# Performance work log

Measured on AMD Instinct MI355X. Metric: run time of the kernel, lower is better.

Reference implementation:

```python
import jax, jax.numpy as jnp
import numpy as np

B, N, R = 16, 128, 16256
OBJ_D, REL_D, EFF_D = 64, 32, 100
REL_HID, OBJ_HID = 150, 100


def setup_inputs() -> dict:
    key = jax.random.key(0)
    ks = jax.random.split(key, 20)
    inp = {
        "objects": jax.random.normal(ks[0], (B, N, OBJ_D), jnp.float32),
        "sender_relations": jax.random.uniform(ks[1], (B, N, R), jnp.float32),
        "receiver_relations": jax.random.uniform(ks[2], (B, N, R), jnp.float32),
        "relation_info": jax.random.normal(ks[3], (B, R, REL_D), jnp.float32),
    }
    rel_in = 2 * OBJ_D + REL_D  # 160
    def lin(k, fin, fout):
        s = 1.0 / np.sqrt(fin)
        kw, kb = jax.random.split(k)
        w = jax.random.uniform(kw, (fin, fout), jnp.float32, -s, s)
        b = jax.random.uniform(kb, (fout,), jnp.float32, -s, s)
        return w, b
    inp["rw1"], inp["rb1"] = lin(ks[4], rel_in, REL_HID)
    inp["rw2"], inp["rb2"] = lin(ks[5], REL_HID, REL_HID)
    inp["rw3"], inp["rb3"] = lin(ks[6], REL_HID, REL_HID)
    inp["rw4"], inp["rb4"] = lin(ks[7], REL_HID, EFF_D)
    inp["ow1"], inp["ob1"] = lin(ks[8], OBJ_D + EFF_D, OBJ_HID)
    inp["ow2"], inp["ob2"] = lin(ks[9], OBJ_HID, 1)
    return inp


def reference(objects, sender_relations, receiver_relations, relation_info,
              rw1, rb1, rw2, rb2, rw3, rb3, rw4, rb4, ow1, ob1, ow2, ob2):
    # gather: [B,R,N] @ [B,N,D] -> [B,R,D]
    senders = jnp.einsum("bnr,bnd->brd", sender_relations, objects)
    receivers = jnp.einsum("bnr,bnd->brd", receiver_relations, objects)
    x = jnp.concatenate([senders, receivers, relation_info], axis=2)  # [B,R,160]
    h = jax.nn.relu(x @ rw1 + rb1)
    h = jax.nn.relu(h @ rw2 + rb2)
    h = jax.nn.relu(h @ rw3 + rb3)
    effects = jax.nn.relu(h @ rw4 + rb4)  # [B,R,EFF_D]
    # scatter: [B,N,R] @ [B,R,E] -> [B,N,E]
    effect_receivers = jnp.einsum("bnr,bre->bne", receiver_relations, effects)
    y = jnp.concatenate([objects, effect_receivers], axis=2)  # [B,N,OBJ_D+EFF_D]
    y = y.reshape(-1, y.shape[-1])  # [B*N, 164]
    predicted = jax.nn.relu(y @ ow1 + ob1) @ ow2 + ob2  # [B*N, 1]
    return jax.nn.sigmoid(predicted)
```

## Files before the change

### kernel.cpp

```cpp
#include <hip/hip_runtime.h>
#include <math.h>

#define B_    16
#define N_    128
#define R_    16256
#define OBJD  64
#define RELD  32
#define EFFD  100
#define HID   150
#define MT    64
#define NTILE (R_ / MT)

typedef __bf16 bf16x8 __attribute__((ext_vector_type(8)));
typedef float  f32x4  __attribute__((ext_vector_type(4)));
typedef unsigned int  uint4v __attribute__((ext_vector_type(4)));
typedef unsigned short u16;
typedef unsigned long long u64;

#define MFMA(a,b,c) (c) = __builtin_amdgcn_mfma_f32_16x16x32_bf16((a), (b), (c), 0, 0, 0)

#define EF_FLOATS (B_*N_*EFFD)
#define A1_ELEMS  (B_*160*288)
#define W2_ELEMS  (160*160)
#define W4_ELEMS  (128*160)
#define U_A1H 0
#define U_A1L (U_A1H + A1_ELEMS)
#define U_W2H (U_A1L + A1_ELEMS)
#define U_W2L (U_W2H + W2_ELEMS)
#define U_W3H (U_W2L + W2_ELEMS)
#define U_W3L (U_W3H + W2_ELEMS)
#define U_W4H (U_W3L + W2_ELEMS)
#define U_W4L (U_W4H + W4_ELEMS)

__device__ __forceinline__ u16 bfh(float x){
    unsigned u = __float_as_uint(x);
    return (u16)((u + 0x7FFFu + ((u >> 16) & 1u)) >> 16);
}
__device__ __forceinline__ float bff(u16 h){ return __uint_as_float(((unsigned)h) << 16); }
__device__ __forceinline__ void split2(float x, u16 &h, u16 &l){
    h = bfh(x);
    l = bfh(x - bff(h));
}
__device__ __forceinline__ u64 pack4(const u16 h[4]){
    return (u64)((unsigned)h[0] | ((unsigned)h[1] << 16))
         | ((u64)((unsigned)h[2] | ((unsigned)h[3] << 16)) << 32);
}

__global__ __launch_bounds__(128) void k0a(const float* __restrict__ obj,
                                           const float* __restrict__ rw1,
                                           u16* __restrict__ A1H, u16* __restrict__ A1L){
    const int j = blockIdx.x;
    const int b = blockIdx.y;
    const int n = threadIdx.x;
    float s = 0.f, rc = 0.f;
    if (j < HID){
        const float* o = obj + ((size_t)b*N_ + n)*OBJD;
#pragma unroll
        for (int d = 0; d < OBJD; ++d){
            const float ov = o[d];
            s  += ov * rw1[d*HID + j];
            rc += ov * rw1[(OBJD + d)*HID + j];
        }
    }
    const size_t base = ((size_t)b*160 + j)*288;
    const int pos = (n & ~31) + (((((n >> 3) & 3) ^ (j & 3))) << 3) + (n & 7);
    u16 h, l;
    split2(s, h, l);  A1H[base + pos] = h;        A1L[base + pos] = l;
    split2(rc, h, l); A1H[base + 128 + pos] = h;  A1L[base + 128 + pos] = l;
    if (n < RELD){
        const float v = (j < HID) ? rw1[(2*OBJD + n)*HID + j] : 0.f;
        const int p2 = 256 + ((((n >> 3) & 3) ^ (j & 3)) << 3) + (n & 7);
        split2(v, h, l); A1H[base + p2] = h; A1L[base + p2] = l;
    }
}

__global__ __launch_bounds__(160) void k0b(const float* __restrict__ rw2,
                                           const float* __restrict__ rw3,
                                           const float* __restrict__ rw4,
                                           u16* W2H, u16* W2L, u16* W3H, u16* W3L,
                                           u16* W4H, u16* W4L){
    const int out = blockIdx.x;
    const int m   = blockIdx.y;
    const int k   = threadIdx.x;
    const int pos = (k & ~31) + ((((k >> 3) & 3) ^ (out & 3)) << 3) + (k & 7);
    u16 h, l;
    if (m == 2){
        if (out >= 128) return;
        const float v = (out < EFFD && k < HID) ? rw4[k*EFFD + out] : 0.f;
        split2(v, h, l);
        W4H[out*160 + pos] = h; W4L[out*160 + pos] = l;
    } else {
        const float* W = (m == 0) ? rw2 : rw3;
        u16* DH = (m == 0) ? W2H : W3H;
        u16* DL = (m == 0) ? W2L : W3L;
        const float v = (out < HID && k < HID) ? W[k*HID + out] : 0.f;
        split2(v, h, l);
        DH[out*160 + pos] = h; DL[out*160 + pos] = l;
    }
}

#define ACT_H 0
#define ACT_L 20480
#define WA_H  40960
#define WA_L  51200
#define BS_H  61440
#define BS_L  65536
#define RRE_H 0
#define RRE_L 20480
#define EFF_H 40960
#define EFF_L 61440
#define SMEM_BYTES 81920

__global__ __launch_bounds__(256, 2) void k1(
    const float* __restrict__ SR, const float* __restrict__ RR, const float* __restrict__ REL,
    const float* __restrict__ rb1, const float* __restrict__ rb2,
    const float* __restrict__ rb3, const float* __restrict__ rb4,
    const u16* __restrict__ UA, float* __restrict__ EF){

    __shared__ __align__(16) unsigned char smem[SMEM_BYTES];

    const int t    = threadIdx.x;
    const int wid  = t >> 6;
    const int lane = t & 63;
    const int lr   = lane & 15;
    const int lg   = lane >> 4;
    const int wr   = wid >> 1;
    const int wc   = wid & 1;
    const int b    = blockIdx.y;
    const int r0   = blockIdx.x * MT;

    const u16* A1Hb = UA + U_A1H + (size_t)b*160*288;
    const u16* A1Lb = UA + U_A1L + (size_t)b*160*288;

    u64 wh[5], wl[5];
    float bsv[8];

    auto wload = [&](const u16* GH, const u16* GL, int KW, int pieces, int c){
#pragma unroll
        for (int q = 0; q < 5; ++q){
            const int p = t + 256*q;
            if (p < pieces){
                const size_t off = (size_t)(p >> 3)*KW + c*32 + (p & 7)*4;
                wh[q] = *(const u64*)(GH + off);
                wl[q] = *(const u64*)(GL + off);
            }
        }
    };
    auto wwrite = [&](int pieces){
#pragma unroll
        for (int q = 0; q < 5; ++q){
            const int p = t + 256*q;
            if (p < pieces){
                *(u64*)(smem + WA_H + p*8) = wh[q];
                *(u64*)(smem + WA_L + p*8) = wl[q];
            }
        }
    };
    auto bs_load_srr = [&](int c){
        const float* SRC = (c < 4) ? SR : RR;
        const float* base = SRC + ((size_t)b*N_ + (c & 3)*32 + wid*8)*R_ + r0 + lane;
#pragma unroll
        for (int q = 0; q < 8; ++q) bsv[q] = base[(size_t)q * R_];
    };
    auto bs_load_rel = [&](){
        const int rel = t >> 2, gq = t & 3;
        const float* src = REL + ((size_t)b*R_ + r0 + rel)*RELD + gq*8;
#pragma unroll
        for (int q = 0; q < 8; ++q) bsv[q] = src[q];
    };
    auto bs_pack_write = [&](int rel, int gr){
        unsigned ph[4], pl[4];
#pragma unroll
        for (int i = 0; i < 4; ++i){
            u16 h0, l0, h1, l1;
            split2(bsv[2*i],   h0, l0);
            split2(bsv[2*i+1], h1, l1);
            ph[i] = (unsigned)h0 | ((unsigned)h1 << 16);
            pl[i] = (unsigned)l0 | ((unsigned)l1 << 16);
        }
        const int off = (rel*4 + (gr ^ (rel & 3))) * 16;
        uint4v H; H[0]=ph[0]; H[1]=ph[1]; H[2]=ph[2]; H[3]=ph[3];
        uint4v L; L[0]=pl[0]; L[1]=pl[1]; L[2]=pl[2]; L[3]=pl[3];
        *(uint4v*)(smem + BS_H + off) = H;
        *(uint4v*)(smem + BS_L + off) = L;
    };
    auto RD = [&](int off) -> bf16x8 {
        return __builtin_bit_cast(bf16x8, *(const uint4v*)(smem + off));
    };

    f32x4 acc[5][2];

    auto epi_act = [&](){
#pragma unroll
        for (int mb = 0; mb < 5; ++mb){
            const int out0 = wr*80 + mb*16 + lg*4;
            const int g = out0 >> 3;
#pragma unroll
            for (int nb = 0; nb < 2; ++nb){
                const int rel = wc*32 + nb*16 + lr;
                const int g2 = (g & ~3) | ((g & 3) ^ (rel & 3));
                u16 h[4], l[4];
#pragma unroll
                for (int r = 0; r < 4; ++r){
                    const float v = fmaxf(acc[mb][nb][r], 0.f);
                    split2(v, h[r], l[r]);
                }
                const int ob = (rel*20 + g2)*16 + (out0 & 7)*2;
                *(u64*)(smem + ACT_H + ob) = pack4(h);
                *(u64*)(smem + ACT_L + ob) = pack4(l);
            }
        }
    };

    {
#pragma unroll
        for (int mb = 0; mb < 5; ++mb){
            const int o0 = wr*80 + mb*16 + lg*4;
            f32x4 bv;
#pragma unroll
            for (int r = 0; r < 4; ++r) bv[r] = (o0 + r < HID) ? rb1[o0 + r] : 0.f;
            acc[mb][0] = bv; acc[mb][1] = bv;
        }
        wload(A1Hb, A1Lb, 288, 1280, 0);
        bs_load_srr(0);
        wwrite(1280);
        bs_pack_write(lane, wid);
        __syncthreads();
        for (int c = 0; c < 9; ++c){
            if (c < 8){
                wload(A1Hb, A1Lb, 288, 1280, c + 1);
                if (c + 1 < 8) bs_load_srr(c + 1); else bs_load_rel();
            }
            bf16x8 ah[5], al[5], bh[2], bl[2];
#pragma unroll
            for (int mb = 0; mb < 5; ++mb){
                const int row = wr*80 + mb*16 + lr;
                const int off = (row*4 + (lg ^ (row & 3))) * 16;
                ah[mb] = RD(WA_H + off); al[mb] = RD(WA_L + off);
            }
#pragma unroll
            for (int nb = 0; nb < 2; ++nb){
                const int rel = wc*32 + nb*16 + lr;
                const int off = (rel*4 + (lg ^ (rel & 3))) * 16;
                bh[nb] = RD(BS_H + off); bl[nb] = RD(BS_L + off);
            }
            __syncthreads();
#pragma unroll
            for (int mb = 0; mb < 5; ++mb)
#pragma unroll
            for (int nb = 0; nb < 2; ++nb){
                MFMA(ah[mb], bh[nb], acc[mb][nb]);
                MFMA(ah[mb], bl[nb], acc[mb][nb]);
                MFMA(al[mb], bh[nb], acc[mb][nb]);
            }
            if (c < 8){
                wwrite(1280);
                if (c + 1 < 8) bs_pack_write(lane, wid); else bs_pack_write(t >> 2, t & 3);
            }
            __syncthreads();
        }
        epi_act();
        __syncthreads();
    }

    {
        const u16* WHs[2] = { UA + U_W2H, UA + U_W3H };
        const u16* WLs[2] = { UA + U_W2L, UA + U_W3L };
        const float* RBs[2] = { rb2, rb3 };
        for (int L = 0; L < 2; ++L){
#pragma unroll
            for (int mb = 0; mb < 5; ++mb){
                const int o0 = wr*80 + mb*16 + lg*4;
                f32x4 bv;
#pragma unroll
                for (int r = 0; r < 4; ++r) bv[r] = (o0 + r < HID) ? RBs[L][o0 + r] : 0.f;
                acc[mb][0] = bv; acc[mb][1] = bv;
            }
            wload(WHs[L], WLs[L], 160, 1280, 0);
            wwrite(1280);
            __syncthreads();
            for (int c = 0; c < 5; ++c){
                if (c < 4) wload(WHs[L], WLs[L], 160, 1280, c + 1);
                bf16x8 ah[5], al[5], bh[2], bl[2];
#pragma unroll
                for (int mb = 0; mb < 5; ++mb){
                    const int row = wr*80 + mb*16 + lr;
                    const int off = (row*4 + (lg ^ (row & 3))) * 16;
                    ah[mb] = RD(WA_H + off); al[mb] = RD(WA_L + off);
                }
#pragma unroll
                for (int nb = 0; nb < 2; ++nb){
                    const int rel = wc*32 + nb*16 + lr;
                    const int off = (rel*20 + c*4 + (lg ^ (rel & 3))) * 16;
                    bh[nb] = RD(ACT_H + off); bl[nb] = RD(ACT_L + off);
                }
                __syncthreads();
#pragma unroll
                for (int mb = 0; mb < 5; ++mb)
#pragma unroll
                for (int nb = 0; nb < 2; ++nb){
                    MFMA(ah[mb], bh[nb], acc[mb][nb]);
                    MFMA(ah[mb], bl[nb], acc[mb][nb]);
                    MFMA(al[mb], bh[nb], acc[mb][nb]);
                }
                if (c < 4) wwrite(1280);
                __syncthreads();
            }
            epi_act();
            __syncthreads();
        }
    }

    {
        f32x4 a4[2][4];
#pragma unroll
        for (int eb = 0; eb < 4; ++eb){
            const int e = wc*64 + eb*16 + lr;
            const float bvv = (e < EFFD) ? rb4[e] : 0.f;
            f32x4 v; v[0]=bvv; v[1]=bvv; v[2]=bvv; v[3]=bvv;
            a4[0][eb] = v; a4[1][eb] = v;
        }
        float vrr[32];
        {
            const int n = t >> 1, half = t & 1;
            const float* src = RR + ((size_t)b*N_ + n)*R_ + r0 + half*32;
#pragma unroll
            for (int q = 0; q < 8; ++q){
                const float4 f = *(const float4*)(src + q*4);
                vrr[q*4+0] = f.x; vrr[q*4+1] = f.y; vrr[q*4+2] = f.z; vrr[q*4+3] = f.w;
            }
        }
        const u16* W4Hp = UA + U_W4H;
        const u16* W4Lp = UA + U_W4L;
        wload(W4Hp, W4Lp, 160, 1024, 0);
        wwrite(1024);
        __syncthreads();
        for (int c = 0; c < 5; ++c){
            if (c < 4) wload(W4Hp, W4Lp, 160, 1024, c + 1);
            bf16x8 ah[2], al[2], bh[4], bl[4];
#pragma unroll
            for (int rb = 0; rb < 2; ++rb){
                const int row = wr*32 + rb*16 + lr;
                const int off = (row*20 + c*4 + (lg ^ (row & 3))) * 16;
                ah[rb] = RD(ACT_H + off); al[rb] = RD(ACT_L + off);
            }
#pragma unroll
            for (int eb = 0; eb < 4; ++eb){
                const int row = wc*64 + eb*16 + lr;
                const int off = (row*4 + (lg ^ (row & 3))) * 16;
                bh[eb] = RD(WA_H + off); bl[eb] = RD(WA_L + off);
            }
            __syncthreads();
#pragma unroll
            for (int rb = 0; rb < 2; ++rb)
#pragma unroll
            for (int eb = 0; eb < 4; ++eb){
                MFMA(ah[rb], bh[eb], a4[rb][eb]);
                MFMA(ah[rb], bl[eb], a4[rb][eb]);
                MFMA(al[rb], bh[eb], a4[rb][eb]);
            }
            if (c < 4) wwrite(1024);
            __syncthreads();
        }
#pragma unroll
        for (int rb = 0; rb < 2; ++rb){
            const int rel0 = wr*32 + rb*16 + lg*4;
            const int g = rel0 >> 3;
#pragma unroll
            for (int eb = 0; eb < 4; ++eb){
                const int e = wc*64 + eb*16 + lr;
                const int g2 = (g & ~3) | ((g & 3) ^ (e & 3));
                u16 h[4], l[4];
#pragma unroll
                for (int r = 0; r < 4; ++r){
                    const float v = fmaxf(a4[rb][eb][r], 0.f);
                    split2(v, h[r], l[r]);
                }
                const int ob = (e*10 + g2)*16 + (rel0 & 7)*2;
                *(u64*)(smem + EFF_H + ob) = pack4(h);
                *(u64*)(smem + EFF_L + ob) = pack4(l);
            }
        }
        {
            const int n = t >> 1, half = t & 1;
#pragma unroll
            for (int gq = 0; gq < 4; ++gq){
                unsigned ph[4], pl[4];
#pragma unroll
                for (int i = 0; i < 4; ++i){
                    u16 h0, l0, h1, l1;
                    split2(vrr[gq*8 + 2*i],     h0, l0);
                    split2(vrr[gq*8 + 2*i + 1], h1, l1);
                    ph[i] = (unsigned)h0 | ((unsigned)h1 << 16);
                    pl[i] = (unsigned)l0 | ((unsigned)l1 << 16);
                }
                const int off = (n*10 + half*4 + (gq ^ (n & 3))) * 16;
                uint4v H; H[0]=ph[0]; H[1]=ph[1]; H[2]=ph[2]; H[3]=ph[3];
                uint4v L; L[0]=pl[0]; L[1]=pl[1]; L[2]=pl[2]; L[3]=pl[3];
                *(uint4v*)(smem + RRE_H + off) = H;
                *(uint4v*)(smem + RRE_L + off) = L;
            }
        }
        __syncthreads();
    }

    {
        f32x4 ae[4][4];
#pragma unroll
        for (int nb = 0; nb < 4; ++nb)
#pragma unroll
        for (int eb = 0; eb < 4; ++eb){
            ae[nb][eb][0]=0.f; ae[nb][eb][1]=0.f; ae[nb][eb][2]=0.f; ae[nb][eb][3]=0.f;
        }
#pragma unroll
        for (int ks = 0; ks < 2; ++ks){
            bf16x8 rh[4], rl[4], eh[4], el[4];
#pragma unroll
            for (int nb = 0; nb < 4; ++nb){
                const int row = wr*64 + nb*16 + lr;
                const int off = (row*10 + ks*4 + (lg ^ (row & 3))) * 16;
                rh[nb] = RD(RRE_H + off); rl[nb] = RD(RRE_L + off);
            }
#pragma unroll
            for (int eb = 0; eb < 4; ++eb){
                const int row = wc*64 + eb*16 + lr;
                const int off = (row*10 + ks*4 + (lg ^ (row & 3))) * 16;
                eh[eb] = RD(EFF_H + off); el[eb] = RD(EFF_L + off);
            }
#pragma unroll
            for (int nb = 0; nb < 4; ++nb)
#pragma unroll
            for (int eb = 0; eb < 4; ++eb){
                MFMA(rh[nb], eh[eb], ae[nb][eb]);
                MFMA(rh[nb], el[eb], ae[nb][eb]);
                MFMA(rl[nb], eh[eb], ae[nb][eb]);
            }
        }
        float* EFb = EF + (size_t)b*N_*EFFD;
#pragma unroll
        for (int eb = 0; eb < 4; ++eb){
            const int e = wc*64 + eb*16 + lr;
            if (e < EFFD){
#pragma unroll
                for (int nb = 0; nb < 4; ++nb){
                    const int n0 = wr*64 + nb*16 + lg*4;
#pragma unroll
                    for (int r = 0; r < 4; ++r)
                        atomicAdd(&EFb[(size_t)(n0 + r)*EFFD + e], ae[nb][eb][r]);
                }
            }
        }
    }
}

__global__ __launch_bounds__(128) void k3_out(
    const float* __restrict__ EF, const float* __restrict__ obj,
    const float* __restrict__ ow1, const float* __restrict__ ob1,
    const float* __restrict__ ow2, const float* __restrict__ ob2,
    float* __restrict__ out) {
    __shared__ float y[OBJD + EFFD];
    __shared__ float red[128];
    const int bn = blockIdx.x;
    const int t  = threadIdx.x;
    if (t < OBJD) y[t] = obj[(size_t)bn * OBJD + t];
    if (t < EFFD) y[OBJD + t] = EF[(size_t)bn * EFFD + t];
    __syncthreads();
    float prod = 0.f;
    if (t < 100) {
        float h = ob1[t];
#pragma unroll
        for (int k = 0; k < OBJD + EFFD; ++k) h += y[k] * ow1[k * 100 + t];
        prod = fmaxf(h, 0.f) * ow2[t];
    }
    red[t] = prod;
    __syncthreads();
#pragma unroll
    for (int s = 64; s > 0; s >>= 1) {
        if (t < s) red[t] += red[t + s];
        __syncthreads();
    }
    if (t == 0) {
        const float x = red[0] + ob2[0];
        float sig;
        if (x >= 0.f) sig = 1.f / (1.f + expf(-x));
        else { const float e = expf(x); sig = e / (1.f + e); }
        out[bn] = sig;
    }
}

extern "C" void kernel_launch(void* const* d_in, const int* in_sizes, int n_in,
                              void* d_out, int out_size, void* d_ws, size_t ws_size,
                              hipStream_t stream) {
    const float* obj = (const float*)d_in[0];
    const float* SR  = (const float*)d_in[1];
    const float* RR  = (const float*)d_in[2];
    const float* REL = (const float*)d_in[3];
    const float* rw1 = (const float*)d_in[4];
    const float* rb1 = (const float*)d_in[5];
    const float* rw2 = (const float*)d_in[6];
    const float* rb2 = (const float*)d_in[7];
    const float* rw3 = (const float*)d_in[8];
    const float* rb3 = (const float*)d_in[9];
    const float* rw4 = (const float*)d_in[10];
    const float* rb4 = (const float*)d_in[11];
    const float* ow1 = (const float*)d_in[12];
    const float* ob1 = (const float*)d_in[13];
    const float* ow2 = (const float*)d_in[14];
    const float* ob2 = (const float*)d_in[15];
    float* out = (float*)d_out;
    float* ws  = (float*)d_ws;

    float* EF = ws;
    u16*   UA = (u16*)(ws + EF_FLOATS);

    hipMemsetAsync(EF, 0, (size_t)EF_FLOATS * sizeof(float), stream);

    k0a<<<dim3(160, B_), dim3(128), 0, stream>>>(obj, rw1, UA + U_A1H, UA + U_A1L);
    k0b<<<dim3(160, 3), dim3(160), 0, stream>>>(rw2, rw3, rw4,
                                                UA + U_W2H, UA + U_W2L,
                                                UA + U_W3H, UA + U_W3L,
                                                UA + U_W4H, UA + U_W4L);
    k1<<<dim3(NTILE, B_), dim3(256), 0, stream>>>(SR, RR, REL, rb1, rb2, rb3, rb4,
                                                  (const u16*)UA, EF);
    k3_out<<<dim3(B_ * N_), dim3(128), 0, stream>>>(EF, obj, ow1, ob1, ow2, ob2, out);
}
```

Baseline: 800.9 us.

## Double-buffer weight and operand LDS tiles and retune XOR swizzle patterns

Weight and relation-operand staging buffers in shared memory become two ping-pong buffers per GEMM stage, so the barrier between reading fragments and writing the next chunk is dropped, leaving one sync per k-step. The swizzle functions also change from XOR with row&3 to XOR with (row>>1)&3 or (row>>2)&3, which is meant to cut LDS bank conflicts for the row strides used. The risk is more LDS layout pressure within the existing 80 KB footprint, plus the correctness of reusing the ACT/EFF regions once the extra barriers are gone.

```diff
diff --git a/kernel.cpp b/kernel.cpp
--- a/kernel.cpp
+++ b/kernel.cpp
@@ -18,6 +18,9 @@
 typedef unsigned long long u64;
 
 #define MFMA(a,b,c) (c) = __builtin_amdgcn_mfma_f32_16x16x32_bf16((a), (b), (c), 0, 0, 0)
+
+#define SWZA(r,g) ((g) ^ (((r) >> 1) & 3))
+#define SWZE(r,g) ((g) ^ (((r) >> 2) & 3))
 
 #define EF_FLOATS (B_*N_*EFFD)
 #define A1_ELEMS  (B_*160*288)
@@ -63,13 +66,13 @@
         }
     }
     const size_t base = ((size_t)b*160 + j)*288;
-    const int pos = (n & ~31) + (((((n >> 3) & 3) ^ (j & 3))) << 3) + (n & 7);
+    const int pos = (n & ~31) + (SWZA(j, (n >> 3) & 3) << 3) + (n & 7);
     u16 h, l;
     split2(s, h, l);  A1H[base + pos] = h;        A1L[base + pos] = l;
     split2(rc, h, l); A1H[base + 128 + pos] = h;  A1L[base + 128 + pos] = l;
     if (n < RELD){
         const float v = (j < HID) ? rw1[(2*OBJD + n)*HID + j] : 0.f;
-        const int p2 = 256 + ((((n >> 3) & 3) ^ (j & 3)) << 3) + (n & 7);
+        const int p2 = 256 + (SWZA(j, (n >> 3) & 3) << 3) + (n & 7);
         split2(v, h, l); A1H[base + p2] = h; A1L[base + p2] = l;
     }
 }
@@ -82,7 +85,7 @@
     const int out = blockIdx.x;
     const int m   = blockIdx.y;
     const int k   = threadIdx.x;
-    const int pos = (k & ~31) + ((((k >> 3) & 3) ^ (out & 3)) << 3) + (k & 7);
+    const int pos = (k & ~31) + (SWZA(out, (k >> 3) & 3) << 3) + (k & 7);
     u16 h, l;
     if (m == 2){
         if (out >= 128) return;
@@ -99,12 +102,12 @@
     }
 }
 
+#define G1WB(i) ((i) * 20480)
+#define G1BS(i) (61440 + (i) * 8192)
 #define ACT_H 0
 #define ACT_L 20480
-#define WA_H  40960
-#define WA_L  51200
-#define BS_H  61440
-#define BS_L  65536
+#define G2WB(i) (40960 + (i) * 20480)
+#define G4WB(i) (40960 + (i) * 16384)
 #define RRE_H 0
 #define RRE_L 20480
 #define EFF_H 40960
@@ -146,13 +149,14 @@
             }
         }
     };
-    auto wwrite = [&](int pieces){
+    auto wwrite = [&](int base, int pieces){
+        const int loff = pieces * 8;
 #pragma unroll
         for (int q = 0; q < 5; ++q){
             const int p = t + 256*q;
             if (p < pieces){
-                *(u64*)(smem + WA_H + p*8) = wh[q];
-                *(u64*)(smem + WA_L + p*8) = wl[q];
+                *(u64*)(smem + base + p*8)        = wh[q];
+                *(u64*)(smem + base + loff + p*8) = wl[q];
             }
         }
     };
@@ -168,7 +172,7 @@
 #pragma unroll
         for (int q = 0; q < 8; ++q) bsv[q] = src[q];
     };
-    auto bs_pack_write = [&](int rel, int gr){
+    auto bs_pack_write = [&](int base, int rel, int gr){
         unsigned ph[4], pl[4];
 #pragma unroll
         for (int i = 0; i < 4; ++i){
@@ -178,11 +182,11 @@
             ph[i] = (unsigned)h0 | ((unsigned)h1 << 16);
             pl[i] = (unsigned)l0 | ((unsigned)l1 << 16);
         }
-        const int off = (rel*4 + (gr ^ (rel & 3))) * 16;
+        const int off = (rel*4 + SWZA(rel, gr)) * 16;
         uint4v H; H[0]=ph[0]; H[1]=ph[1]; H[2]=ph[2]; H[3]=ph[3];
         uint4v L; L[0]=pl[0]; L[1]=pl[1]; L[2]=pl[2]; L[3]=pl[3];
-        *(uint4v*)(smem + BS_H + off) = H;
-        *(uint4v*)(smem + BS_L + off) = L;
+        *(uint4v*)(smem + base + off)        = H;
+        *(uint4v*)(smem + base + 4096 + off) = L;
     };
     auto RD = [&](int off) -> bf16x8 {
         return __builtin_bit_cast(bf16x8, *(const uint4v*)(smem + off));
@@ -198,7 +202,7 @@
 #pragma unroll
             for (int nb = 0; nb < 2; ++nb){
                 const int rel = wc*32 + nb*16 + lr;
-                const int g2 = (g & ~3) | ((g & 3) ^ (rel & 3));
+                const int g2 = (g & ~3) | SWZA(rel, g & 3);
                 u16 h[4], l[4];
 #pragma unroll
                 for (int r = 0; r < 4; ++r){
@@ -223,28 +227,28 @@
         }
         wload(A1Hb, A1Lb, 288, 1280, 0);
         bs_load_srr(0);
-        wwrite(1280);
-        bs_pack_write(lane, wid);
+        wwrite(G1WB(0), 1280);
+        bs_pack_write(G1BS(0), lane, wid);
         __syncthreads();
         for (int c = 0; c < 9; ++c){
             if (c < 8){
                 wload(A1Hb, A1Lb, 288, 1280, c + 1);
                 if (c + 1 < 8) bs_load_srr(c + 1); else bs_load_rel();
             }
+            const int wb = G1WB(c & 1), bb = G1BS(c & 1);
             bf16x8 ah[5], al[5], bh[2], bl[2];
 #pragma unroll
             for (int mb = 0; mb < 5; ++mb){
                 const int row = wr*80 + mb*16 + lr;
-                const int off = (row*4 + (lg ^ (row & 3))) * 16;
-                ah[mb] = RD(WA_H + off); al[mb] = RD(WA_L + off);
+                const int off = (row*4 + SWZA(row, lg)) * 16;
+                ah[mb] = RD(wb + off); al[mb] = RD(wb + 10240 + off);
             }
 #pragma unroll
             for (int nb = 0; nb < 2; ++nb){
                 const int rel = wc*32 + nb*16 + lr;
-                const int off = (rel*4 + (lg ^ (rel & 3))) * 16;
-                bh[nb] = RD(BS_H + off); bl[nb] = RD(BS_L + off);
-            }
-            __syncthreads();
+                const int off = (rel*4 + SWZA(rel, lg)) * 16;
+                bh[nb] = RD(bb + off); bl[nb] = RD(bb + 4096 + off);
+            }
 #pragma unroll
             for (int mb = 0; mb < 5; ++mb)
 #pragma unroll
@@ -254,13 +258,13 @@
                 MFMA(al[mb], bh[nb], acc[mb][nb]);
             }
             if (c < 8){
-                wwrite(1280);
-                if (c + 1 < 8) bs_pack_write(lane, wid); else bs_pack_write(t >> 2, t & 3);
+                wwrite(G1WB((c + 1) & 1), 1280);
+                if (c + 1 < 8) bs_pack_write(G1BS((c + 1) & 1), lane, wid);
+                else           bs_pack_write(G1BS((c + 1) & 1), t >> 2, t & 3);
             }
             __syncthreads();
         }
         epi_act();
-        __syncthreads();
     }
 
     {
@@ -277,24 +281,24 @@
                 acc[mb][0] = bv; acc[mb][1] = bv;
             }
             wload(WHs[L], WLs[L], 160, 1280, 0);
-            wwrite(1280);
+            wwrite(G2WB(0), 1280);
             __syncthreads();
             for (int c = 0; c < 5; ++c){
                 if (c < 4) wload(WHs[L], WLs[L], 160, 1280, c + 1);
+                const int wb = G2WB(c & 1);
                 bf16x8 ah[5], al[5], bh[2], bl[2];
 #pragma unroll
                 for (int mb = 0; mb < 5; ++mb){
                     const int row = wr*80 + mb*16 + lr;
-                    const int off = (row*4 + (lg ^ (row & 3))) * 16;
-                    ah[mb] = RD(WA_H + off); al[mb] = RD(WA_L + off);
+                    const int off = (row*4 + SWZA(row, lg)) * 16;
+                    ah[mb] = RD(wb + off); al[mb] = RD(wb + 10240 + off);
                 }
 #pragma unroll
                 for (int nb = 0; nb < 2; ++nb){
                     const int rel = wc*32 + nb*16 + lr;
-                    const int off = (rel*20 + c*4 + (lg ^ (rel & 3))) * 16;
+                    const int off = (rel*20 + c*4 + SWZA(rel, lg)) * 16;
                     bh[nb] = RD(ACT_H + off); bl[nb] = RD(ACT_L + off);
                 }
-                __syncthreads();
 #pragma unroll
                 for (int mb = 0; mb < 5; ++mb)
 #pragma unroll
@@ -303,11 +307,10 @@
                     MFMA(ah[mb], bl[nb], acc[mb][nb]);
                     MFMA(al[mb], bh[nb], acc[mb][nb]);
                 }
-                if (c < 4) wwrite(1280);
+                if (c < 4) wwrite(G2WB((c + 1) & 1), 1280);
                 __syncthreads();
             }
             epi_act();
-            __syncthreads();
         }
     }
 
@@ -333,24 +336,24 @@
         const u16* W4Hp = UA + U_W4H;
         const u16* W4Lp = UA + U_W4L;
         wload(W4Hp, W4Lp, 160, 1024, 0);
-        wwrite(1024);
+        wwrite(G4WB(0), 1024);
         __syncthreads();
         for (int c = 0; c < 5; ++c){
             if (c < 4) wload(W4Hp, W4Lp, 160, 1024, c + 1);
+            const int wb = G4WB(c & 1);
             bf16x8 ah[2], al[2], bh[4], bl[4];
 #pragma unroll
             for (int rb = 0; rb < 2; ++rb){
                 const int row = wr*32 + rb*16 + lr;
-                const int off = (row*20 + c*4 + (lg ^ (row & 3))) * 16;
+                const int off = (row*20 + c*4 + SWZA(row, lg)) * 16;
                 ah[rb] = RD(ACT_H + off); al[rb] = RD(ACT_L + off);
             }
 #pragma unroll
             for (int eb = 0; eb < 4; ++eb){
                 const int row = wc*64 + eb*16 + lr;
-                const int off = (row*4 + (lg ^ (row & 3))) * 16;
-                bh[eb] = RD(WA_H + off); bl[eb] = RD(WA_L + off);
-            }
-            __syncthreads();
+                const int off = (row*4 + SWZA(row, lg)) * 16;
+                bh[eb] = RD(wb + off); bl[eb] = RD(wb + 8192 + off);
+            }
 #pragma unroll
             for (int rb = 0; rb < 2; ++rb)
 #pragma unroll
@@ -359,7 +362,7 @@
                 MFMA(ah[rb], bl[eb], a4[rb][eb]);
                 MFMA(al[rb], bh[eb], a4[rb][eb]);
             }
-            if (c < 4) wwrite(1024);
+            if (c < 4) wwrite(G4WB((c + 1) & 1), 1024);
             __syncthreads();
         }
 #pragma unroll
@@ -369,7 +372,7 @@
 #pragma unroll
             for (int eb = 0; eb < 4; ++eb){
                 const int e = wc*64 + eb*16 + lr;
-                const int g2 = (g & ~3) | ((g & 3) ^ (e & 3));
+                const int g2 = (g & ~3) | SWZE(e, g & 3);
                 u16 h[4], l[4];
 #pragma unroll
                 for (int r = 0; r < 4; ++r){
@@ -394,7 +397,7 @@
                     ph[i] = (unsigned)h0 | ((unsigned)h1 << 16);
                     pl[i] = (unsigned)l0 | ((unsigned)l1 << 16);
                 }
-                const int off = (n*10 + half*4 + (gq ^ (n & 3))) * 16;
+                const int off = (n*10 + half*4 + SWZE(n, gq)) * 16;
                 uint4v H; H[0]=ph[0]; H[1]=ph[1]; H[2]=ph[2]; H[3]=ph[3];
                 uint4v L; L[0]=pl[0]; L[1]=pl[1]; L[2]=pl[2]; L[3]=pl[3];
                 *(uint4v*)(smem + RRE_H + off) = H;
@@ -418,13 +421,13 @@
 #pragma unroll
             for (int nb = 0; nb < 4; ++nb){
                 const int row = wr*64 + nb*16 + lr;
-                const int off = (row*10 + ks*4 + (lg ^ (row & 3))) * 16;
+                const int off = (row*10 + ks*4 + SWZE(row, lg)) * 16;
                 rh[nb] = RD(RRE_H + off); rl[nb] = RD(RRE_L + off);
             }
 #pragma unroll
             for (int eb = 0; eb < 4; ++eb){
                 const int row = wc*64 + eb*16 + lr;
-                const int off = (row*10 + ks*4 + (lg ^ (row & 3))) * 16;
+                const int off = (row*10 + ks*4 + SWZE(row, lg)) * 16;
                 eh[eb] = RD(EFF_H + off); el[eb] = RD(EFF_L + off);
             }
 #pragma unroll
```

After: 796.4 us. Within noise of the previous version (-0.6%).
